# Performance work log

Measured on AMD Instinct MI355X. Metric: run time of the kernel, lower is better.

The kernel has to match this reference:

```python
import jax, jax.numpy as jnp
import numpy as np

NUM_GRAPHS = 256
LAMBDA = 0.01


def setup_inputs() -> dict:
    key = jax.random.key(0)
    k1, k2, k3, k4, k5 = jax.random.split(key, 5)
    N, D, E = 100000, 64, 1200000
    logits = jax.random.normal(k1, (NUM_GRAPHS, 10), dtype=jnp.float32)
    labels = jax.random.randint(k2, (NUM_GRAPHS,), 0, 10, dtype=jnp.int64)
    x = jax.random.normal(k3, (N, D), dtype=jnp.float32)
    edge_index = jax.random.randint(k4, (2, E), 0, N, dtype=jnp.int64)
    batch = jnp.sort(jax.random.randint(k5, (N,), 0, NUM_GRAPHS, dtype=jnp.int64))
    return {"logits": logits, "labels": labels, "x": x,
            "edge_index": edge_index, "batch": batch}


def reference(logits, labels, x, edge_index, batch):
    # cross-entropy (mean over graphs)
    logp = jax.nn.log_softmax(logits, axis=-1)
    ce_loss = -jnp.mean(jnp.take_along_axis(logp, labels[:, None], axis=1))

    # Dirichlet energy
    row, col = edge_index[0], edge_index[1]
    N = x.shape[0]
    ones_e = jnp.ones(row.shape, dtype=x.dtype)
    deg = jax.ops.segment_sum(ones_e, row, num_segments=N)          # [N]
    deg_inv_sqrt = jnp.where(deg > 0, jax.lax.rsqrt(jnp.where(deg > 0, deg, 1.0)), 0.0)
    norm = deg_inv_sqrt[row] * deg_inv_sqrt[col]                    # [E]
    diff = x[row] - x[col]                                          # [E, D]
    sq = jnp.sum(diff * diff, axis=1)                               # [E]
    energy_e = norm * sq

    seg = batch[row]                                                # graph id per edge
    energy_sum = jax.ops.segment_sum(energy_e, seg, num_segments=NUM_GRAPHS)
    edge_counts = jax.ops.segment_sum(ones_e, seg, num_segments=NUM_GRAPHS)
    edge_counts = jnp.clip(edge_counts, 1.0, None)
    smoothness_loss = jnp.mean(energy_sum / edge_counts)

    return ce_loss + LAMBDA * smoothness_loss
```

## Files before the change

### kernel.cpp

```cpp
#include <hip/hip_runtime.h>
#include <math.h>

#define NUM_GRAPHS 256
#define LAMBDA 0.01f

typedef int   v4i __attribute__((ext_vector_type(4)));
typedef float v4f __attribute__((ext_vector_type(4)));

__global__ void k_deg_sq(const int* __restrict__ row, const int* __restrict__ col,
                         const float4* __restrict__ x4, float* __restrict__ deg,
                         float* __restrict__ sq, int E) {
    const int lane   = threadIdx.x & 63;
    const int lane16 = lane & 15;
    const int wave   = (blockIdx.x * blockDim.x + threadIdx.x) >> 6;
    const int nwaves = (gridDim.x * blockDim.x) >> 6;
    const int gi     = (lane >> 4);
    const int E16    = E >> 4;

    for (int t = wave; t < E16; t += nwaves) {
        const int ebase = t * 16 + gi * 4;

        v4i rv = __builtin_nontemporal_load((const v4i*)(row + ebase));
        v4i cv = __builtin_nontemporal_load((const v4i*)(col + ebase));
        const int r0 = rv[0], r1 = rv[1], r2 = rv[2], r3 = rv[3];
        const int c0 = cv[0], c1 = cv[1], c2 = cv[2], c3 = cv[3];

        float4 a0 = x4[(long)r0 * 16 + lane16];
        float4 b0 = x4[(long)c0 * 16 + lane16];
        float4 a1 = x4[(long)r1 * 16 + lane16];
        float4 b1 = x4[(long)c1 * 16 + lane16];
        float4 a2 = x4[(long)r2 * 16 + lane16];
        float4 b2 = x4[(long)c2 * 16 + lane16];
        float4 a3 = x4[(long)r3 * 16 + lane16];
        float4 b3 = x4[(long)c3 * 16 + lane16];

        float dx, dy, dz, dw;
        dx = a0.x - b0.x; dy = a0.y - b0.y; dz = a0.z - b0.z; dw = a0.w - b0.w;
        float s0 = dx * dx + dy * dy + dz * dz + dw * dw;
        dx = a1.x - b1.x; dy = a1.y - b1.y; dz = a1.z - b1.z; dw = a1.w - b1.w;
        float s1 = dx * dx + dy * dy + dz * dz + dw * dw;
        dx = a2.x - b2.x; dy = a2.y - b2.y; dz = a2.z - b2.z; dw = a2.w - b2.w;
        float s2 = dx * dx + dy * dy + dz * dz + dw * dw;
        dx = a3.x - b3.x; dy = a3.y - b3.y; dz = a3.z - b3.z; dw = a3.w - b3.w;
        float s3 = dx * dx + dy * dy + dz * dz + dw * dw;

        s0 += __shfl_xor(s0, 1); s1 += __shfl_xor(s1, 1);
        s2 += __shfl_xor(s2, 1); s3 += __shfl_xor(s3, 1);
        s0 += __shfl_xor(s0, 2); s1 += __shfl_xor(s1, 2);
        s2 += __shfl_xor(s2, 2); s3 += __shfl_xor(s3, 2);
        s0 += __shfl_xor(s0, 4); s1 += __shfl_xor(s1, 4);
        s2 += __shfl_xor(s2, 4); s3 += __shfl_xor(s3, 4);
        s0 += __shfl_xor(s0, 8); s1 += __shfl_xor(s1, 8);
        s2 += __shfl_xor(s2, 8); s3 += __shfl_xor(s3, 8);

        if (lane16 == 0) {
            v4f sv;
            sv[0] = s0; sv[1] = s1; sv[2] = s2; sv[3] = s3;
            __builtin_nontemporal_store(sv, (v4f*)(sq + ebase));
        } else if (lane16 == 1) {
            atomicAdd(&deg[r0], 1.0f);
        } else if (lane16 == 2) {
            atomicAdd(&deg[r1], 1.0f);
        } else if (lane16 == 3) {
            atomicAdd(&deg[r2], 1.0f);
        } else if (lane16 == 4) {
            atomicAdd(&deg[r3], 1.0f);
        }
    }

    for (int e = (E16 << 4) + wave; e < E; e += nwaves) {
        int r = row[e], c = col[e];
        float4 a = x4[(long)r * 16 + lane16];
        float4 b = x4[(long)c * 16 + lane16];
        float dx = a.x - b.x, dy = a.y - b.y, dz = a.z - b.z, dw = a.w - b.w;
        float s = dx * dx + dy * dy + dz * dz + dw * dw;
        s += __shfl_xor(s, 1);
        s += __shfl_xor(s, 2);
        s += __shfl_xor(s, 4);
        s += __shfl_xor(s, 8);
        if (lane == 0) sq[e] = s;
        if (lane == 1) atomicAdd(&deg[r], 1.0f);
    }
}

template <bool PACK>
__global__ void k_dis(float* __restrict__ deg_dis, const int* __restrict__ batch,
                      float* __restrict__ cnt, float2* __restrict__ pk, int N) {
    int i = blockIdx.x * blockDim.x + threadIdx.x;
    bool valid = (i < N);
    float d = valid ? deg_dis[i] : 0.0f;
    int g = valid ? batch[i] : -1;
    float dis = (d > 0.0f) ? rsqrtf(d) : 0.0f;
    if (valid) {
        deg_dis[i] = dis;
        if (PACK) pk[i] = make_float2(dis, __int_as_float(g));
    }

    int gmin = g, gmax = g;
    #pragma unroll
    for (int m = 1; m < 64; m <<= 1) {
        gmin = min(gmin, __shfl_xor(gmin, m));
        gmax = max(gmax, __shfl_xor(gmax, m));
    }
    if (gmin == gmax && gmin >= 0) {
        float s = d;
        #pragma unroll
        for (int m = 1; m < 64; m <<= 1) s += __shfl_xor(s, m);
        if ((threadIdx.x & 63) == 0) atomicAdd(&cnt[g], s);
    } else if (valid) {
        atomicAdd(&cnt[g], d);
    }
}

__global__ void k_bin(const int* __restrict__ row, const int* __restrict__ col,
                      const float* __restrict__ sq, const float2* __restrict__ pk,
                      float* __restrict__ g_energy, int E) {
    __shared__ float lbin[NUM_GRAPHS];
    lbin[threadIdx.x] = 0.0f;
    __syncthreads();

    const int i = blockIdx.x * blockDim.x + threadIdx.x;
    const int stride = gridDim.x * blockDim.x;
    const int E4 = E >> 2;
    const v4i* r4 = (const v4i*)row;
    const v4i* c4 = (const v4i*)col;
    const v4f* s4 = (const v4f*)sq;

    for (int k = i; k < E4; k += stride) {
        v4i r = __builtin_nontemporal_load(&r4[k]);
        v4i c = __builtin_nontemporal_load(&c4[k]);
        v4f s = __builtin_nontemporal_load(&s4[k]);
        float2 pr0 = pk[r[0]], pr1 = pk[r[1]], pr2 = pk[r[2]], pr3 = pk[r[3]];
        float2 pc0 = pk[c[0]], pc1 = pk[c[1]], pc2 = pk[c[2]], pc3 = pk[c[3]];
        atomicAdd(&lbin[__float_as_int(pr0.y)], pr0.x * pc0.x * s[0]);
        atomicAdd(&lbin[__float_as_int(pr1.y)], pr1.x * pc1.x * s[1]);
        atomicAdd(&lbin[__float_as_int(pr2.y)], pr2.x * pc2.x * s[2]);
        atomicAdd(&lbin[__float_as_int(pr3.y)], pr3.x * pc3.x * s[3]);
    }
    for (int e = (E4 << 2) + i; e < E; e += stride) {
        float2 pr = pk[row[e]], pc = pk[col[e]];
        atomicAdd(&lbin[__float_as_int(pr.y)], pr.x * pc.x * sq[e]);
    }

    __syncthreads();
    float v = lbin[threadIdx.x];
    if (v != 0.0f) atomicAdd(&g_energy[threadIdx.x], v);
}

__global__ void k_bin_fb(const int* __restrict__ row, const int* __restrict__ col,
                         const float* __restrict__ sq, const float* __restrict__ dis,
                         const int* __restrict__ batch, float* __restrict__ g_energy,
                         int E) {
    __shared__ float lbin[NUM_GRAPHS];
    lbin[threadIdx.x] = 0.0f;
    __syncthreads();

    const int i = blockIdx.x * blockDim.x + threadIdx.x;
    const int stride = gridDim.x * blockDim.x;
    const int E4 = E >> 2;
    const v4i* r4 = (const v4i*)row;
    const v4i* c4 = (const v4i*)col;
    const v4f* s4 = (const v4f*)sq;

    for (int k = i; k < E4; k += stride) {
        v4i r = __builtin_nontemporal_load(&r4[k]);
        v4i c = __builtin_nontemporal_load(&c4[k]);
        v4f s = __builtin_nontemporal_load(&s4[k]);
        #pragma unroll
        for (int j = 0; j < 4; ++j) {
            float nr = dis[r[j]] * dis[c[j]];
            atomicAdd(&lbin[batch[r[j]]], nr * s[j]);
        }
    }
    for (int e = (E4 << 2) + i; e < E; e += stride) {
        int r = row[e], c = col[e];
        atomicAdd(&lbin[batch[r]], dis[r] * dis[c] * sq[e]);
    }

    __syncthreads();
    float v = lbin[threadIdx.x];
    if (v != 0.0f) atomicAdd(&g_energy[threadIdx.x], v);
}

__global__ void k_deg(const int* __restrict__ row, float* __restrict__ deg, int E) {
    const int i = blockIdx.x * blockDim.x + threadIdx.x;
    const int stride = gridDim.x * blockDim.x;
    for (int e = i; e < E; e += stride) atomicAdd(&deg[row[e]], 1.0f);
}

__global__ void k_energy(const int* __restrict__ row, const int* __restrict__ col,
                         const float4* __restrict__ x4, const float* __restrict__ dis,
                         const int* __restrict__ batch, float* __restrict__ g_energy,
                         int E) {
    __shared__ float lbin[NUM_GRAPHS];
    lbin[threadIdx.x] = 0.0f;
    __syncthreads();

    const int lane16 = threadIdx.x & 15;
    const int group = (blockIdx.x * blockDim.x + threadIdx.x) >> 4;
    const int ngroups = (gridDim.x * blockDim.x) >> 4;

    for (int e = group; e < E; e += ngroups) {
        int r = row[e];
        int c = col[e];
        float4 a = x4[(long)r * 16 + lane16];
        float4 b = x4[(long)c * 16 + lane16];
        float nr = dis[r] * dis[c];
        int g = batch[r];
        float dx = a.x - b.x, dy = a.y - b.y, dz = a.z - b.z, dw = a.w - b.w;
        float s = dx * dx + dy * dy + dz * dz + dw * dw;
        s += __shfl_xor(s, 1);
        s += __shfl_xor(s, 2);
        s += __shfl_xor(s, 4);
        s += __shfl_xor(s, 8);
        if (lane16 == 0) atomicAdd(&lbin[g], nr * s);
    }

    __syncthreads();
    float v = lbin[threadIdx.x];
    if (v != 0.0f) atomicAdd(&g_energy[threadIdx.x], v);
}

__global__ void k_final(const float* __restrict__ logits, const int* __restrict__ labels,
                        const float* __restrict__ g_energy, const float* __restrict__ cnt,
                        float* __restrict__ out) {
    const int t = threadIdx.x;
    const float* lg = logits + t * 10;

    float m = -INFINITY;
    #pragma unroll
    for (int j = 0; j < 10; ++j) m = fmaxf(m, lg[j]);
    float sum = 0.0f;
    #pragma unroll
    for (int j = 0; j < 10; ++j) sum += expf(lg[j] - m);
    float lse = m + logf(sum);
    float ce = lse - lg[labels[t]];

    float sm = g_energy[t] / fmaxf(cnt[t], 1.0f);

    float v = ce + LAMBDA * sm;
    #pragma unroll
    for (int mk = 1; mk < 64; mk <<= 1) v += __shfl_xor(v, mk);

    __shared__ float wsum[4];
    if ((t & 63) == 0) wsum[t >> 6] = v;
    __syncthreads();
    if (t == 0) out[0] = (wsum[0] + wsum[1] + wsum[2] + wsum[3]) * (1.0f / 256.0f);
}

extern "C" void kernel_launch(void* const* d_in, const int* in_sizes, int n_in,
                              void* d_out, int out_size, void* d_ws, size_t ws_size,
                              hipStream_t stream) {
    const float* logits = (const float*)d_in[0];
    const int* labels   = (const int*)d_in[1];
    const float* x      = (const float*)d_in[2];
    const int* edge_idx = (const int*)d_in[3];
    const int* batch    = (const int*)d_in[4];

    const int N = in_sizes[2] / 64;
    const int E = in_sizes[3] / 2;

    float*  deg_dis  = (float*)d_ws;
    float*  g_energy = deg_dis + N;
    float*  cnt      = g_energy + NUM_GRAPHS;
    float*  sq       = cnt + NUM_GRAPHS;
    float2* pk       = (float2*)(sq + E);

    (void)hipMemsetAsync(d_ws, 0, (size_t)(N + 2 * NUM_GRAPHS) * sizeof(float), stream);

    const int* row = edge_idx;
    const int* col = edge_idx + E;

    const size_t base_floats = (size_t)N + 2 * NUM_GRAPHS;
    const size_t need_sq  = (base_floats + (size_t)E) * sizeof(float);
    const size_t need_pk  = need_sq + (size_t)2 * N * sizeof(float);
    const int bin_blocks = (E / 4 + 255) / 256;

    if (ws_size >= need_pk) {
        k_deg_sq<<<2048, 256, 0, stream>>>(row, col, (const float4*)x, deg_dis, sq, E);
        k_dis<true><<<(N + 255) / 256, 256, 0, stream>>>(deg_dis, batch, cnt, pk, N);
        k_bin<<<bin_blocks, 256, 0, stream>>>(row, col, sq, pk, g_energy, E);
    } else if (ws_size >= need_sq) {
        k_deg_sq<<<2048, 256, 0, stream>>>(row, col, (const float4*)x, deg_dis, sq, E);
        k_dis<false><<<(N + 255) / 256, 256, 0, stream>>>(deg_dis, batch, cnt, pk, N);
        k_bin_fb<<<bin_blocks, 256, 0, stream>>>(row, col, sq, deg_dis, batch,
                                                 g_energy, E);
    } else {
        k_deg<<<2048, 256, 0, stream>>>(row, deg_dis, E);
        k_dis<false><<<(N + 255) / 256, 256, 0, stream>>>(deg_dis, batch, cnt, pk, N);
        k_energy<<<2048, 256, 0, stream>>>(row, col, (const float4*)x, deg_dis, batch,
                                           g_energy, E);
    }
    k_final<<<1, 256, 0, stream>>>(logits, labels, g_energy, cnt, (float*)d_out);
}
```

Baseline: 227.5 us.

## Convert node features to bf16 before gathering and fuse workspace zeroing

Adds a conversion kernel that writes a bf16 copy of x into workspace and, in the same launch, zeroes the degree and per-graph accumulators, replacing the memset. The edge kernel then gathers 128-byte bf16 rows with 8 lanes per edge instead of 256-byte fp32 rows with 16 lanes, halving gather traffic. k_bin now launches a fixed 512 blocks. Rounding x to bf16 before differencing lowers precision of the squared distances, and the extra conversion pass adds a full read of x plus a write of the bf16 copy.

After: 204.8 us. 10.0% less time.

```diff
diff --git a/kernel.cpp b/kernel.cpp
--- a/kernel.cpp
+++ b/kernel.cpp
@@ -4,8 +4,117 @@
 #define NUM_GRAPHS 256
 #define LAMBDA 0.01f
 
-typedef int   v4i __attribute__((ext_vector_type(4)));
-typedef float v4f __attribute__((ext_vector_type(4)));
+typedef int          v4i __attribute__((ext_vector_type(4)));
+typedef float        v4f __attribute__((ext_vector_type(4)));
+typedef unsigned int v4u __attribute__((ext_vector_type(4)));
+typedef unsigned short v8h __attribute__((ext_vector_type(8)));
+
+__device__ __forceinline__ unsigned short f2bf_rne(float f) {
+    unsigned int u = __float_as_uint(f);
+    u = u + 0x7fffu + ((u >> 16) & 1u);
+    return (unsigned short)(u >> 16);
+}
+
+__device__ __forceinline__ float bfdiff_sq(v4u a, v4u b) {
+    float s = 0.0f;
+    #pragma unroll
+    for (int k = 0; k < 4; ++k) {
+        float alo = __uint_as_float(a[k] << 16);
+        float ahi = __uint_as_float(a[k] & 0xffff0000u);
+        float blo = __uint_as_float(b[k] << 16);
+        float bhi = __uint_as_float(b[k] & 0xffff0000u);
+        float d1 = alo - blo;
+        float d2 = ahi - bhi;
+        s += d1 * d1;
+        s += d2 * d2;
+    }
+    return s;
+}
+
+__global__ void k_cvt(const float* __restrict__ x, v8h* __restrict__ xh,
+                      float* __restrict__ zr, int zcount8, long total8) {
+    long j = (long)blockIdx.x * blockDim.x + threadIdx.x;
+    if (j < total8) {
+        const v4f* xp = (const v4f*)(x + j * 8);
+        v4f a = xp[0], b = xp[1];
+        v8h o;
+        o[0] = f2bf_rne(a[0]); o[1] = f2bf_rne(a[1]);
+        o[2] = f2bf_rne(a[2]); o[3] = f2bf_rne(a[3]);
+        o[4] = f2bf_rne(b[0]); o[5] = f2bf_rne(b[1]);
+        o[6] = f2bf_rne(b[2]); o[7] = f2bf_rne(b[3]);
+        __builtin_nontemporal_store(o, xh + j);
+    }
+    if (j < zcount8) {
+        v4f z = {0.0f, 0.0f, 0.0f, 0.0f};
+        v4f* zp = (v4f*)(zr + j * 8);
+        zp[0] = z; zp[1] = z;
+    }
+}
+
+__global__ void k_deg_sq_h(const int* __restrict__ row, const int* __restrict__ col,
+                           const v4u* __restrict__ xh4, float* __restrict__ deg,
+                           float* __restrict__ sq, int E) {
+    const int lane   = threadIdx.x & 63;
+    const int lane8  = lane & 7;
+    const int gi     = lane >> 3;
+    const int wave   = (blockIdx.x * blockDim.x + threadIdx.x) >> 6;
+    const int nwaves = (gridDim.x * blockDim.x) >> 6;
+    const int E32    = E >> 5;
+
+    for (int t = wave; t < E32; t += nwaves) {
+        const int ebase = t * 32 + gi * 4;
+
+        v4i rv = __builtin_nontemporal_load((const v4i*)(row + ebase));
+        v4i cv = __builtin_nontemporal_load((const v4i*)(col + ebase));
+
+        v4u a0 = xh4[(long)rv[0] * 8 + lane8];
+        v4u b0 = xh4[(long)cv[0] * 8 + lane8];
+        v4u a1 = xh4[(long)rv[1] * 8 + lane8];
+        v4u b1 = xh4[(long)cv[1] * 8 + lane8];
+        v4u a2 = xh4[(long)rv[2] * 8 + lane8];
+        v4u b2 = xh4[(long)cv[2] * 8 + lane8];
+        v4u a3 = xh4[(long)rv[3] * 8 + lane8];
+        v4u b3 = xh4[(long)cv[3] * 8 + lane8];
+
+        float s0 = bfdiff_sq(a0, b0);
+        float s1 = bfdiff_sq(a1, b1);
+        float s2 = bfdiff_sq(a2, b2);
+        float s3 = bfdiff_sq(a3, b3);
+
+        s0 += __shfl_xor(s0, 1); s1 += __shfl_xor(s1, 1);
+        s2 += __shfl_xor(s2, 1); s3 += __shfl_xor(s3, 1);
+        s0 += __shfl_xor(s0, 2); s1 += __shfl_xor(s1, 2);
+        s2 += __shfl_xor(s2, 2); s3 += __shfl_xor(s3, 2);
+        s0 += __shfl_xor(s0, 4); s1 += __shfl_xor(s1, 4);
+        s2 += __shfl_xor(s2, 4); s3 += __shfl_xor(s3, 4);
+
+        if (lane8 == 0) {
+            v4f sv;
+            sv[0] = s0; sv[1] = s1; sv[2] = s2; sv[3] = s3;
+            __builtin_nontemporal_store(sv, (v4f*)(sq + ebase));
+        } else if (lane8 == 1) {
+            atomicAdd(&deg[rv[0]], 1.0f);
+        } else if (lane8 == 2) {
+            atomicAdd(&deg[rv[1]], 1.0f);
+        } else if (lane8 == 3) {
+            atomicAdd(&deg[rv[2]], 1.0f);
+        } else if (lane8 == 4) {
+            atomicAdd(&deg[rv[3]], 1.0f);
+        }
+    }
+
+    for (int e = (E32 << 5) + wave; e < E; e += nwaves) {
+        int r = row[e], c = col[e];
+        v4u a = xh4[(long)r * 8 + lane8];
+        v4u b = xh4[(long)c * 8 + lane8];
+        float s = bfdiff_sq(a, b);
+        s += __shfl_xor(s, 1);
+        s += __shfl_xor(s, 2);
+        s += __shfl_xor(s, 4);
+        if (lane == 0) sq[e] = s;
+        if (lane == 8) atomicAdd(&deg[r], 1.0f);
+    }
+}
 
 __global__ void k_deg_sq(const int* __restrict__ row, const int* __restrict__ col,
                          const float4* __restrict__ x4, float* __restrict__ deg,
@@ -22,17 +131,15 @@
 
         v4i rv = __builtin_nontemporal_load((const v4i*)(row + ebase));
         v4i cv = __builtin_nontemporal_load((const v4i*)(col + ebase));
-        const int r0 = rv[0], r1 = rv[1], r2 = rv[2], r3 = rv[3];
-        const int c0 = cv[0], c1 = cv[1], c2 = cv[2], c3 = cv[3];
-
-        float4 a0 = x4[(long)r0 * 16 + lane16];
-        float4 b0 = x4[(long)c0 * 16 + lane16];
-        float4 a1 = x4[(long)r1 * 16 + lane16];
-        float4 b1 = x4[(long)c1 * 16 + lane16];
-        float4 a2 = x4[(long)r2 * 16 + lane16];
-        float4 b2 = x4[(long)c2 * 16 + lane16];
-        float4 a3 = x4[(long)r3 * 16 + lane16];
-        float4 b3 = x4[(long)c3 * 16 + lane16];
+
+        float4 a0 = x4[(long)rv[0] * 16 + lane16];
+        float4 b0 = x4[(long)cv[0] * 16 + lane16];
+        float4 a1 = x4[(long)rv[1] * 16 + lane16];
+        float4 b1 = x4[(long)cv[1] * 16 + lane16];
+        float4 a2 = x4[(long)rv[2] * 16 + lane16];
+        float4 b2 = x4[(long)cv[2] * 16 + lane16];
+        float4 a3 = x4[(long)rv[3] * 16 + lane16];
+        float4 b3 = x4[(long)cv[3] * 16 + lane16];
 
         float dx, dy, dz, dw;
         dx = a0.x - b0.x; dy = a0.y - b0.y; dz = a0.z - b0.z; dw = a0.w - b0.w;
@@ -58,13 +165,13 @@
             sv[0] = s0; sv[1] = s1; sv[2] = s2; sv[3] = s3;
             __builtin_nontemporal_store(sv, (v4f*)(sq + ebase));
         } else if (lane16 == 1) {
-            atomicAdd(&deg[r0], 1.0f);
+            atomicAdd(&deg[rv[0]], 1.0f);
         } else if (lane16 == 2) {
-            atomicAdd(&deg[r1], 1.0f);
+            atomicAdd(&deg[rv[1]], 1.0f);
         } else if (lane16 == 3) {
-            atomicAdd(&deg[r2], 1.0f);
+            atomicAdd(&deg[rv[2]], 1.0f);
         } else if (lane16 == 4) {
-            atomicAdd(&deg[r3], 1.0f);
+            atomicAdd(&deg[rv[3]], 1.0f);
         }
     }
 
@@ -265,27 +372,36 @@
     float*  cnt      = g_energy + NUM_GRAPHS;
     float*  sq       = cnt + NUM_GRAPHS;
     float2* pk       = (float2*)(sq + E);
-
-    (void)hipMemsetAsync(d_ws, 0, (size_t)(N + 2 * NUM_GRAPHS) * sizeof(float), stream);
+    unsigned short* xh = (unsigned short*)(pk + N);
 
     const int* row = edge_idx;
     const int* col = edge_idx + E;
 
     const size_t base_floats = (size_t)N + 2 * NUM_GRAPHS;
-    const size_t need_sq  = (base_floats + (size_t)E) * sizeof(float);
-    const size_t need_pk  = need_sq + (size_t)2 * N * sizeof(float);
-    const int bin_blocks = (E / 4 + 255) / 256;
-
-    if (ws_size >= need_pk) {
+    const size_t need_sq = (base_floats + (size_t)E) * sizeof(float);
+    const size_t need_pk = need_sq + (size_t)2 * N * sizeof(float);
+    const size_t need_xh = need_pk + (size_t)N * 64 * sizeof(unsigned short);
+
+    if (ws_size >= need_xh) {
+        const long total8 = (long)N * 8;
+        const int zcount8 = (int)((N + 2 * NUM_GRAPHS) / 8);
+        const int cvt_blocks = (int)((total8 + 255) / 256);
+        k_cvt<<<cvt_blocks, 256, 0, stream>>>(x, (v8h*)xh, deg_dis, zcount8, total8);
+        k_deg_sq_h<<<2048, 256, 0, stream>>>(row, col, (const v4u*)xh, deg_dis, sq, E);
+        k_dis<true><<<(N + 255) / 256, 256, 0, stream>>>(deg_dis, batch, cnt, pk, N);
+        k_bin<<<512, 256, 0, stream>>>(row, col, sq, pk, g_energy, E);
+    } else if (ws_size >= need_pk) {
+        (void)hipMemsetAsync(d_ws, 0, (size_t)(N + 2 * NUM_GRAPHS) * sizeof(float), stream);
         k_deg_sq<<<2048, 256, 0, stream>>>(row, col, (const float4*)x, deg_dis, sq, E);
         k_dis<true><<<(N + 255) / 256, 256, 0, stream>>>(deg_dis, batch, cnt, pk, N);
-        k_bin<<<bin_blocks, 256, 0, stream>>>(row, col, sq, pk, g_energy, E);
+        k_bin<<<512, 256, 0, stream>>>(row, col, sq, pk, g_energy, E);
     } else if (ws_size >= need_sq) {
+        (void)hipMemsetAsync(d_ws, 0, (size_t)(N + 2 * NUM_GRAPHS) * sizeof(float), stream);
         k_deg_sq<<<2048, 256, 0, stream>>>(row, col, (const float4*)x, deg_dis, sq, E);
         k_dis<false><<<(N + 255) / 256, 256, 0, stream>>>(deg_dis, batch, cnt, pk, N);
-        k_bin_fb<<<bin_blocks, 256, 0, stream>>>(row, col, sq, deg_dis, batch,
-                                                 g_energy, E);
+        k_bin_fb<<<512, 256, 0, stream>>>(row, col, sq, deg_dis, batch, g_energy, E);
     } else {
+        (void)hipMemsetAsync(d_ws, 0, (size_t)(N + 2 * NUM_GRAPHS) * sizeof(float), stream);
         k_deg<<<2048, 256, 0, stream>>>(row, deg_dis, E);
         k_dis<false><<<(N + 255) / 256, 256, 0, stream>>>(deg_dis, batch, cnt, pk, N);
         k_energy<<<2048, 256, 0, stream>>>(row, col, (const float4*)x, deg_dis, batch,
```
